# Kernel tuning notes

Measured on AMD Instinct MI355X. Metric: run time of the kernel, lower is better.

The kernel has to match this reference:

```python
import jax, jax.numpy as jnp
import numpy as np

N = 512        # n_nodes
S = 64         # state_dim
M = 64         # message_dim
HM = 128       # hidden_unit_message_dim
HR = 128       # hidden_unit_readout_dim
STEPS = 5      # n_steps


def setup_inputs() -> dict:
    key = jax.random.key(0)
    ks = jax.random.split(key, 12)
    def w(k, shape):
        return jax.random.normal(k, shape, jnp.float32) * 0.1  # normal_(0, 0.1)
    gru_bound = 1.0 / np.sqrt(S)  # torch GRUCell default init
    def u(k, shape):
        return jax.random.uniform(k, shape, jnp.float32, -gru_bound, gru_bound)
    return {
        "J": jax.random.normal(ks[0], (N, N), jnp.float32),
        "b": jax.random.normal(ks[1], (N,), jnp.float32),
        # message MLP (weights stored [in, out])
        "mW1": w(ks[2], (2 * S + 3, HM)), "mb1": jnp.zeros((HM,), jnp.float32),
        "mW2": w(ks[3], (HM, HM)),        "mb2": jnp.zeros((HM,), jnp.float32),
        "mW3": w(ks[4], (HM, M)),         "mb3": jnp.zeros((M,), jnp.float32),
        # GRUCell params (torch layout: [3*hidden, in])
        "W_ih": u(ks[5], (3 * S, M)), "b_ih": u(ks[6], (3 * S,)),
        "W_hh": u(ks[7], (3 * S, S)), "b_hh": u(ks[8], (3 * S,)),
        # readout MLP
        "rW1": w(ks[9], (S, HR)),  "rb1": jnp.zeros((HR,), jnp.float32),
        "rW2": w(ks[10], (HR, HR)), "rb2": jnp.zeros((HR,), jnp.float32),
        "rW3": w(ks[11], (HR, 2)),  "rb3": jnp.zeros((2,), jnp.float32),
    }


def reference(J, b, mW1, mb1, mW2, mb2, mW3, mb3,
              W_ih, b_ih, W_hh, b_hh,
              rW1, rb1, rW2, rb2, rW3, rb3):
    n = J.shape[0]
    # split first message layer: input = [h_i, h_j, J_ij, b_i, b_j]
    W_hi, W_hj = mW1[:S], mW1[S:2 * S]
    w_J, w_bi, w_bj = mW1[2 * S], mW1[2 * S + 1], mW1[2 * S + 2]
    # pair-dependent, state-independent part of layer-1 preactivation  [N,N,HM]
    pair_bias = (J[:, :, None] * w_J + b[:, None, None] * w_bi
                 + b[None, :, None] * w_bj + mb1)

    def gru(x, h):
        gx = x @ W_ih.T + b_ih
        gh = h @ W_hh.T + b_hh
        xr, xz, xn = jnp.split(gx, 3, axis=-1)
        hr, hz, hn = jnp.split(gh, 3, axis=-1)
        r = jax.nn.sigmoid(xr + hr)
        z = jax.nn.sigmoid(xz + hz)
        ncand = jnp.tanh(xn + r * hn)
        return (1.0 - z) * ncand + z * h

    def step(h, _):
        pre = (h @ W_hi)[:, None, :] + (h @ W_hj)[None, :, :] + pair_bias  # [N,N,HM]
        h1 = jax.nn.relu(pre)
        h2 = jax.nn.relu(h1 @ mW2 + mb2)       # [N,N,HM]
        msg_ij = h2 @ mW3 + mb3                # [N,N,M]
        msg = msg_ij.sum(axis=0)               # sum over i -> message to j  [N,M]
        return gru(msg, h), None

    h0 = jnp.zeros((n, S), J.dtype)
    hT, _ = jax.lax.scan(step, h0, None, length=STEPS)
    out = jax.nn.relu(hT @ rW1 + rb1)
    out = jax.nn.relu(out @ rW2 + rb2)
    out = out @ rW3 + rb3                      # [N,2]
    return jax.nn.softmax(out, axis=1)
```

## Files before the change

kernel.cpp:

```cpp
#include <hip/hip_runtime.h>
#include <math.h>
#include <stdint.h>

typedef _Float16 half8 __attribute__((ext_vector_type(8)));
typedef float f32x4 __attribute__((ext_vector_type(4)));
typedef float fvec4 __attribute__((ext_vector_type(4)));
typedef uint32_t u32x4 __attribute__((ext_vector_type(4)));

#define NN   512
#define SS   64
#define HMID 128
#define MM   64

__global__ void prep_all_kernel(const float* __restrict__ b,
                                const float* __restrict__ mW1,
                                const float* __restrict__ mb1,
                                const float* __restrict__ W_ih,
                                const float* __restrict__ W_hh,
                                float* __restrict__ hbuf,
                                float* __restrict__ Hi, float* __restrict__ Hj,
                                float* __restrict__ WT_ih,
                                float* __restrict__ WT_hh) {
    int idx = blockIdx.x * 256 + threadIdx.x;
    if (idx < 32768) {
        hbuf[idx] = 0.0f;
    } else if (idx < 32768 + 65536) {
        int j = idx - 32768;
        int node = j >> 7, dm = j & 127;
        float bn = b[node];
        Hi[j] = bn * mW1[129 * HMID + dm];
        Hj[j] = bn * mW1[130 * HMID + dm] + mb1[dm];
    } else if (idx < 32768 + 65536 + 12288) {
        int j = idx - 32768 - 65536;
        int g = j / 64, k = j % 64;
        WT_ih[k * 192 + g] = W_ih[j];
        WT_hh[k * 192 + g] = W_hh[j];
    }
}

__global__ __launch_bounds__(256) void main_step_kernel(
    const float* __restrict__ Hi, const float* __restrict__ Hj,
    const float* __restrict__ J, const float* __restrict__ wJ_g,
    const float* __restrict__ mW2, const float* __restrict__ mb2,
    const float* __restrict__ mW3, float* __restrict__ msg,
    float* __restrict__ partial, int use_partial) {

    __shared__ __align__(16) _Float16 H1h[2][32 * 128];
    __shared__ __align__(16) _Float16 H1l[2][32 * 128];

    const int t   = threadIdx.x;
    const int w   = t >> 6;
    const int l   = t & 63;
    const int l16 = l & 15;
    const int lg  = l >> 4;

    const int j0 = (blockIdx.x & 31) * 16;
    const int ig = blockIdx.x >> 5;

    const int lj = t >> 4;
    const int c  = t & 15;
    fvec4 hjv0 = *(const fvec4*)&Hj[(j0 + lj) * HMID + c * 8];
    fvec4 hjv1 = *(const fvec4*)&Hj[(j0 + lj) * HMID + c * 8 + 4];
    fvec4 wjv0 = *(const fvec4*)&wJ_g[c * 8];
    fvec4 wjv1 = *(const fvec4*)&wJ_g[c * 8 + 4];

    half8 w2h[2][4], w2l[2][4];
    float mb2v[2];
    #pragma unroll
    for (int nb = 0; nb < 2; ++nb) {
        int col = w * 32 + nb * 16 + l16;
        mb2v[nb] = mb2[col];
        #pragma unroll
        for (int kb = 0; kb < 4; ++kb)
            #pragma unroll
            for (int i = 0; i < 8; ++i) {
                int k = kb * 32 + lg * 8 + i;
                float wv = mW2[k * HMID + col];
                _Float16 hh = (_Float16)wv;
                w2h[nb][kb][i] = hh;
                w2l[nb][kb][i] = (_Float16)(wv - (float)hh);
            }
    }

    auto do_pre = [&](int tt, _Float16* __restrict__ dsth,
                      _Float16* __restrict__ dstl) {
        int i0 = (ig * 8 + tt) * 2;
        #pragma unroll
        for (int it = 0; it < 2; ++it) {
            int p = it * 16 + lj;
            float Jw = J[(i0 + it) * NN + j0 + lj];
            fvec4 hi0 = *(const fvec4*)&Hi[(i0 + it) * HMID + c * 8];
            fvec4 hi1 = *(const fvec4*)&Hi[(i0 + it) * HMID + c * 8 + 4];
            half8 hvh, hvl;
            #pragma unroll
            for (int u = 0; u < 4; ++u) {
                float v0 = hi0[u] + hjv0[u] + Jw * wjv0[u];
                float v1 = hi1[u] + hjv1[u] + Jw * wjv1[u];
                v0 = v0 > 0.f ? v0 : 0.f;
                v1 = v1 > 0.f ? v1 : 0.f;
                _Float16 g0 = (_Float16)v0, g1 = (_Float16)v1;
                hvh[u]     = g0;
                hvh[u + 4] = g1;
                hvl[u]     = (_Float16)(v0 - (float)g0);
                hvl[u + 4] = (_Float16)(v1 - (float)g1);
            }
            int addr = p * 128 + ((c ^ lj) << 3);
            *(half8*)&dsth[addr] = hvh;
            *(half8*)&dstl[addr] = hvl;
        }
    };

    do_pre(0, H1h[0], H1l[0]);
    __syncthreads();

    float sacc[2][4];
    #pragma unroll
    for (int nb = 0; nb < 2; ++nb)
        #pragma unroll
        for (int q = 0; q < 4; ++q) sacc[nb][q] = 0.f;

    for (int tt = 0; tt < 8; ++tt) {
        const _Float16* srch = H1h[tt & 1];
        const _Float16* srcl = H1l[tt & 1];
        if (tt < 7) do_pre(tt + 1, H1h[(tt + 1) & 1], H1l[(tt + 1) & 1]);

        f32x4 acc[2][2];
        #pragma unroll
        for (int mb = 0; mb < 2; ++mb)
            #pragma unroll
            for (int nb = 0; nb < 2; ++nb)
                acc[mb][nb] = (f32x4){0.f, 0.f, 0.f, 0.f};
        #pragma unroll
        for (int kb = 0; kb < 4; ++kb) {
            #pragma unroll
            for (int mb = 0; mb < 2; ++mb) {
                int row = mb * 16 + l16;
                int base = row * 128 + (((kb * 4 + lg) ^ l16) << 3);
                half8 ah = *(const half8*)&srch[base];
                half8 al = *(const half8*)&srcl[base];
                #pragma unroll
                for (int nb = 0; nb < 2; ++nb) {
                    acc[mb][nb] = __builtin_amdgcn_mfma_f32_16x16x32_f16(
                        ah, w2h[nb][kb], acc[mb][nb], 0, 0, 0);
                    acc[mb][nb] = __builtin_amdgcn_mfma_f32_16x16x32_f16(
                        al, w2h[nb][kb], acc[mb][nb], 0, 0, 0);
                    acc[mb][nb] = __builtin_amdgcn_mfma_f32_16x16x32_f16(
                        ah, w2l[nb][kb], acc[mb][nb], 0, 0, 0);
                }
            }
        }
        #pragma unroll
        for (int mb = 0; mb < 2; ++mb)
            #pragma unroll
            for (int nb = 0; nb < 2; ++nb)
                #pragma unroll
                for (int q = 0; q < 4; ++q) {
                    float v = acc[mb][nb][q] + mb2v[nb];
                    sacc[nb][q] += (v > 0.f ? v : 0.f);
                }
        __syncthreads();
    }

    uint32_t* S32 = (uint32_t*)&H1h[0][0];
    #pragma unroll
    for (int nb = 0; nb < 2; ++nb)
        #pragma unroll
        for (int q = 0; q < 4; ++q) {
            int j = lg * 4 + q;
            int colc = w * 32 + nb * 16 + l16;
            float s = sacc[nb][q];
            _Float16 hh = (_Float16)s;
            _Float16 ll = (_Float16)(s - (float)hh);
            uint16_t uh = __builtin_bit_cast(uint16_t, hh);
            uint16_t ul = __builtin_bit_cast(uint16_t, ll);
            S32[j * 128 + (colc ^ ((j & 7) << 2))] =
                (uint32_t)uh | ((uint32_t)ul << 16);
        }
    half8 w3h_[4], w3l_[4];
    {
        int col = w * 16 + l16;
        #pragma unroll
        for (int kb = 0; kb < 4; ++kb)
            #pragma unroll
            for (int i = 0; i < 8; ++i) {
                int k = kb * 32 + lg * 8 + i;
                float wv = mW3[k * MM + col];
                _Float16 hh = (_Float16)wv;
                w3h_[kb][i] = hh;
                w3l_[kb][i] = (_Float16)(wv - (float)hh);
            }
    }
    __syncthreads();

    f32x4 accD = (f32x4){0.f, 0.f, 0.f, 0.f};
    #pragma unroll
    for (int kb = 0; kb < 4; ++kb) {
        int row = l16;
        int sw = (row & 7) << 2;
        int cc = kb * 32 + lg * 8;
        const uint32_t* bp = &S32[row * 128];
        u32x4 A = *(const u32x4*)&bp[cc ^ sw];
        u32x4 B = *(const u32x4*)&bp[(cc + 4) ^ sw];
        union { uint32_t wd[4]; half8 hv; } Ah, Al;
        Ah.wd[0] = __builtin_amdgcn_perm(A[1], A[0], 0x05040100u);
        Ah.wd[1] = __builtin_amdgcn_perm(A[3], A[2], 0x05040100u);
        Ah.wd[2] = __builtin_amdgcn_perm(B[1], B[0], 0x05040100u);
        Ah.wd[3] = __builtin_amdgcn_perm(B[3], B[2], 0x05040100u);
        Al.wd[0] = __builtin_amdgcn_perm(A[1], A[0], 0x07060302u);
        Al.wd[1] = __builtin_amdgcn_perm(A[3], A[2], 0x07060302u);
        Al.wd[2] = __builtin_amdgcn_perm(B[1], B[0], 0x07060302u);
        Al.wd[3] = __builtin_amdgcn_perm(B[3], B[2], 0x07060302u);
        accD = __builtin_amdgcn_mfma_f32_16x16x32_f16(Ah.hv, w3h_[kb], accD,
                                                      0, 0, 0);
        accD = __builtin_amdgcn_mfma_f32_16x16x32_f16(Al.hv, w3h_[kb], accD,
                                                      0, 0, 0);
        accD = __builtin_amdgcn_mfma_f32_16x16x32_f16(Ah.hv, w3l_[kb], accD,
                                                      0, 0, 0);
    }

    {
        int m = w * 16 + l16;
        #pragma unroll
        for (int q = 0; q < 4; ++q) {
            int j = j0 + lg * 4 + q;
            if (use_partial)
                partial[ig * (NN * MM) + j * MM + m] = accD[q];
            else
                atomicAdd(&msg[j * MM + m], accD[q]);
        }
    }
}

__global__ __launch_bounds__(256) void gru_kernel(
    float* __restrict__ msg, const float* __restrict__ partial,
    const float* __restrict__ mb3,
    const float* __restrict__ WT_ih, const float* __restrict__ b_ih,
    const float* __restrict__ WT_hh, const float* __restrict__ b_hh,
    float* __restrict__ h, const float* __restrict__ bvec,
    const float* __restrict__ mW1, const float* __restrict__ mb1,
    float* __restrict__ Hi, float* __restrict__ Hj, int lastStep,
    int use_partial,
    const float* __restrict__ rW1, const float* __restrict__ rb1,
    const float* __restrict__ rW2, const float* __restrict__ rb2,
    const float* __restrict__ rW3, const float* __restrict__ rb3,
    float* __restrict__ out) {

    __shared__ float xb[64], hb[64], hnb[64];
    __shared__ float red[4][6][64];
    __shared__ float redx[4][64];
    __shared__ float o1[128], o2[128];
    int t = threadIdx.x;
    int d = t & 63;
    int p = t >> 6;
    int node = blockIdx.x;

    if (use_partial) {
        float s = 0.f;
        #pragma unroll
        for (int g = 0; g < 8; ++g)
            s += partial[(p * 8 + g) * (NN * MM) + node * MM + d];
        redx[p][d] = s;
    }
    __syncthreads();

    if (p == 0) {
        float x;
        if (use_partial) {
            x = redx[0][d] + redx[1][d] + redx[2][d] + redx[3][d]
                + 512.0f * mb3[d];
        } else {
            x = msg[node * MM + d] + 512.0f * mb3[d];
            msg[node * MM + d] = 0.0f;
        }
        xb[d] = x;
        hb[d] = h[node * SS + d];
    }
    __syncthreads();

    {
        float s0 = 0.f, s1 = 0.f, s2 = 0.f, s3 = 0.f, s4 = 0.f, s5 = 0.f;
        int k0 = p * 16;
        for (int kk = 0; kk < 16; ++kk) {
            int k = k0 + kk;
            float xk = xb[k], hk = hb[k];
            const float* wi = &WT_ih[k * 192];
            const float* wh = &WT_hh[k * 192];
            s0 += wi[d] * xk;
            s1 += wi[64 + d] * xk;
            s2 += wi[128 + d] * xk;
            s3 += wh[d] * hk;
            s4 += wh[64 + d] * hk;
            s5 += wh[128 + d] * hk;
        }
        red[p][0][d] = s0; red[p][1][d] = s1; red[p][2][d] = s2;
        red[p][3][d] = s3; red[p][4][d] = s4; red[p][5][d] = s5;
    }
    __syncthreads();

    if (p == 0) {
        float gxr = b_ih[d]       + red[0][0][d] + red[1][0][d] + red[2][0][d] + red[3][0][d];
        float gxz = b_ih[64 + d]  + red[0][1][d] + red[1][1][d] + red[2][1][d] + red[3][1][d];
        float gxn = b_ih[128 + d] + red[0][2][d] + red[1][2][d] + red[2][2][d] + red[3][2][d];
        float ghr = b_hh[d]       + red[0][3][d] + red[1][3][d] + red[2][3][d] + red[3][3][d];
        float ghz = b_hh[64 + d]  + red[0][4][d] + red[1][4][d] + red[2][4][d] + red[3][4][d];
        float ghn = b_hh[128 + d] + red[0][5][d] + red[1][5][d] + red[2][5][d] + red[3][5][d];
        float r = 1.f / (1.f + expf(-(gxr + ghr)));
        float z = 1.f / (1.f + expf(-(gxz + ghz)));
        float nc = tanhf(gxn + r * ghn);
        float hnew = (1.f - z) * nc + z * hb[d];
        h[node * SS + d] = hnew;
        hnb[d] = hnew;
    }
    __syncthreads();

    if (!lastStep) {
        int dm = t & 127;
        int half = t >> 7;
        float bn = bvec[node];
        if (half == 0) {
            float ai = bn * mW1[129 * HMID + dm];
            for (int k = 0; k < 64; ++k)
                ai += hnb[k] * mW1[k * HMID + dm];
            Hi[node * HMID + dm] = ai;
        } else {
            float aj = bn * mW1[130 * HMID + dm] + mb1[dm];
            for (int k = 0; k < 64; ++k)
                aj += hnb[k] * mW1[(64 + k) * HMID + dm];
            Hj[node * HMID + dm] = aj;
        }
    } else {
        if (t < 64) {
            for (int dd = 0; dd < 2; ++dd) {
                int dm = d + dd * 64;
                float a = rb1[dm];
                for (int k = 0; k < 64; ++k) a += hnb[k] * rW1[k * 128 + dm];
                o1[dm] = a > 0.f ? a : 0.f;
            }
        }
        __syncthreads();
        if (t < 64) {
            for (int dd = 0; dd < 2; ++dd) {
                int dm = d + dd * 64;
                float a = rb2[dm];
                for (int k = 0; k < 128; ++k) a += o1[k] * rW2[k * 128 + dm];
                o2[dm] = a > 0.f ? a : 0.f;
            }
        }
        __syncthreads();
        if (t < 64) {
            float p0 = 0.f, p1 = 0.f;
            for (int dd = 0; dd < 2; ++dd) {
                int k = d + dd * 64;
                p0 += o2[k] * rW3[k * 2 + 0];
                p1 += o2[k] * rW3[k * 2 + 1];
            }
            for (int off = 32; off; off >>= 1) {
                p0 += __shfl_xor(p0, off);
                p1 += __shfl_xor(p1, off);
            }
            if (d == 0) {
                p0 += rb3[0];
                p1 += rb3[1];
                float m = fmaxf(p0, p1);
                float e0 = expf(p0 - m), e1 = expf(p1 - m);
                float s = e0 + e1;
                out[node * 2 + 0] = e0 / s;
                out[node * 2 + 1] = e1 / s;
            }
        }
    }
}

extern "C" void kernel_launch(void* const* d_in, const int* in_sizes, int n_in,
                              void* d_out, int out_size, void* d_ws,
                              size_t ws_size, hipStream_t stream) {
    const float* J    = (const float*)d_in[0];
    const float* b    = (const float*)d_in[1];
    const float* mW1  = (const float*)d_in[2];
    const float* mb1  = (const float*)d_in[3];
    const float* mW2  = (const float*)d_in[4];
    const float* mb2  = (const float*)d_in[5];
    const float* mW3  = (const float*)d_in[6];
    const float* mb3  = (const float*)d_in[7];
    const float* W_ih = (const float*)d_in[8];
    const float* b_ih = (const float*)d_in[9];
    const float* W_hh = (const float*)d_in[10];
    const float* b_hh = (const float*)d_in[11];
    const float* rW1  = (const float*)d_in[12];
    const float* rb1  = (const float*)d_in[13];
    const float* rW2  = (const float*)d_in[14];
    const float* rb2  = (const float*)d_in[15];
    const float* rW3  = (const float*)d_in[16];
    const float* rb3  = (const float*)d_in[17];
    float* out = (float*)d_out;

    float* ws    = (float*)d_ws;
    float* hbuf  = ws;
    float* msg   = ws + 32768;
    float* Hi    = ws + 65536;
    float* Hj    = ws + 131072;
    float* WT_ih = ws + 196608;
    float* WT_hh = ws + 208896;
    float* partial = ws + 221184;
    size_t need = (221184 + 1048576) * sizeof(float);
    int use_partial = (ws_size >= need) ? 1 : 0;

    if (!use_partial)
        hipMemsetAsync(msg, 0, NN * MM * sizeof(float), stream);
    prep_all_kernel<<<432, 256, 0, stream>>>(b, mW1, mb1, W_ih, W_hh,
                                             hbuf, Hi, Hj, WT_ih, WT_hh);

    for (int s = 0; s < 5; ++s) {
        main_step_kernel<<<1024, 256, 0, stream>>>(Hi, Hj, J, mW1 + 128 * HMID,
                                                   mW2, mb2, mW3, msg,
                                                   partial, use_partial);
        gru_kernel<<<512, 256, 0, stream>>>(msg, partial, mb3, WT_ih, b_ih,
                                            WT_hh, b_hh, hbuf, b, mW1, mb1,
                                            Hi, Hj, s == 4, use_partial,
                                            rW1, rb1, rW2, rb2, rW3, rb3, out);
    }
}
```

Measured before the change: 194.3 us.

## Compute layer-1 activations directly in MFMA operand registers, drop LDS staging

```diff
diff --git a/kernel.cpp b/kernel.cpp
--- a/kernel.cpp
+++ b/kernel.cpp
@@ -45,8 +45,7 @@
     const float* __restrict__ mW3, float* __restrict__ msg,
     float* __restrict__ partial, int use_partial) {
 
-    __shared__ __align__(16) _Float16 H1h[2][32 * 128];
-    __shared__ __align__(16) _Float16 H1l[2][32 * 128];
+    __shared__ __align__(16) uint32_t S32[16 * 128];
 
     const int t   = threadIdx.x;
     const int w   = t >> 6;
@@ -57,12 +56,15 @@
     const int j0 = (blockIdx.x & 31) * 16;
     const int ig = blockIdx.x >> 5;
 
-    const int lj = t >> 4;
-    const int c  = t & 15;
-    fvec4 hjv0 = *(const fvec4*)&Hj[(j0 + lj) * HMID + c * 8];
-    fvec4 hjv1 = *(const fvec4*)&Hj[(j0 + lj) * HMID + c * 8 + 4];
-    fvec4 wjv0 = *(const fvec4*)&wJ_g[c * 8];
-    fvec4 wjv1 = *(const fvec4*)&wJ_g[c * 8 + 4];
+    fvec4 hjv[4][2], wjv[4][2];
+    #pragma unroll
+    for (int kb = 0; kb < 4; ++kb) {
+        int ko = kb * 32 + lg * 8;
+        hjv[kb][0] = *(const fvec4*)&Hj[(j0 + l16) * HMID + ko];
+        hjv[kb][1] = *(const fvec4*)&Hj[(j0 + l16) * HMID + ko + 4];
+        wjv[kb][0] = *(const fvec4*)&wJ_g[ko];
+        wjv[kb][1] = *(const fvec4*)&wJ_g[ko + 4];
+    }
 
     half8 w2h[2][4], w2l[2][4];
     float mb2v[2];
@@ -82,37 +84,6 @@
             }
     }
 
-    auto do_pre = [&](int tt, _Float16* __restrict__ dsth,
-                      _Float16* __restrict__ dstl) {
-        int i0 = (ig * 8 + tt) * 2;
-        #pragma unroll
-        for (int it = 0; it < 2; ++it) {
-            int p = it * 16 + lj;
-            float Jw = J[(i0 + it) * NN + j0 + lj];
-            fvec4 hi0 = *(const fvec4*)&Hi[(i0 + it) * HMID + c * 8];
-            fvec4 hi1 = *(const fvec4*)&Hi[(i0 + it) * HMID + c * 8 + 4];
-            half8 hvh, hvl;
-            #pragma unroll
-            for (int u = 0; u < 4; ++u) {
-                float v0 = hi0[u] + hjv0[u] + Jw * wjv0[u];
-                float v1 = hi1[u] + hjv1[u] + Jw * wjv1[u];
-                v0 = v0 > 0.f ? v0 : 0.f;
-                v1 = v1 > 0.f ? v1 : 0.f;
-                _Float16 g0 = (_Float16)v0, g1 = (_Float16)v1;
-                hvh[u]     = g0;
-                hvh[u + 4] = g1;
-                hvl[u]     = (_Float16)(v0 - (float)g0);
-                hvl[u + 4] = (_Float16)(v1 - (float)g1);
-            }
-            int addr = p * 128 + ((c ^ lj) << 3);
-            *(half8*)&dsth[addr] = hvh;
-            *(half8*)&dstl[addr] = hvl;
-        }
-    };
-
-    do_pre(0, H1h[0], H1l[0]);
-    __syncthreads();
-
     float sacc[2][4];
     #pragma unroll
     for (int nb = 0; nb < 2; ++nb)
@@ -120,9 +91,9 @@
         for (int q = 0; q < 4; ++q) sacc[nb][q] = 0.f;
 
     for (int tt = 0; tt < 8; ++tt) {
-        const _Float16* srch = H1h[tt & 1];
-        const _Float16* srcl = H1l[tt & 1];
-        if (tt < 7) do_pre(tt + 1, H1h[(tt + 1) & 1], H1l[(tt + 1) & 1]);
+        int i0 = ig * 16 + tt * 2;
+        float J0 = J[i0 * NN + j0 + l16];
+        float J1 = J[(i0 + 1) * NN + j0 + l16];
 
         f32x4 acc[2][2];
         #pragma unroll
@@ -130,25 +101,55 @@
             #pragma unroll
             for (int nb = 0; nb < 2; ++nb)
                 acc[mb][nb] = (f32x4){0.f, 0.f, 0.f, 0.f};
+
         #pragma unroll
         for (int kb = 0; kb < 4; ++kb) {
-            #pragma unroll
-            for (int mb = 0; mb < 2; ++mb) {
-                int row = mb * 16 + l16;
-                int base = row * 128 + (((kb * 4 + lg) ^ l16) << 3);
-                half8 ah = *(const half8*)&srch[base];
-                half8 al = *(const half8*)&srcl[base];
-                #pragma unroll
-                for (int nb = 0; nb < 2; ++nb) {
-                    acc[mb][nb] = __builtin_amdgcn_mfma_f32_16x16x32_f16(
-                        ah, w2h[nb][kb], acc[mb][nb], 0, 0, 0);
-                    acc[mb][nb] = __builtin_amdgcn_mfma_f32_16x16x32_f16(
-                        al, w2h[nb][kb], acc[mb][nb], 0, 0, 0);
-                    acc[mb][nb] = __builtin_amdgcn_mfma_f32_16x16x32_f16(
-                        ah, w2l[nb][kb], acc[mb][nb], 0, 0, 0);
-                }
-            }
-        }
+            int ko = kb * 32 + lg * 8;
+            fvec4 hiA0 = *(const fvec4*)&Hi[i0 * HMID + ko];
+            fvec4 hiA1 = *(const fvec4*)&Hi[i0 * HMID + ko + 4];
+            fvec4 hiB0 = *(const fvec4*)&Hi[(i0 + 1) * HMID + ko];
+            fvec4 hiB1 = *(const fvec4*)&Hi[(i0 + 1) * HMID + ko + 4];
+
+            half8 ah0, al0, ah1, al1;
+            #pragma unroll
+            for (int u = 0; u < 4; ++u) {
+                float vA0 = hiA0[u] + hjv[kb][0][u] + J0 * wjv[kb][0][u];
+                float vA1 = hiA1[u] + hjv[kb][1][u] + J0 * wjv[kb][1][u];
+                float vB0 = hiB0[u] + hjv[kb][0][u] + J1 * wjv[kb][0][u];
+                float vB1 = hiB1[u] + hjv[kb][1][u] + J1 * wjv[kb][1][u];
+                vA0 = vA0 > 0.f ? vA0 : 0.f;
+                vA1 = vA1 > 0.f ? vA1 : 0.f;
+                vB0 = vB0 > 0.f ? vB0 : 0.f;
+                vB1 = vB1 > 0.f ? vB1 : 0.f;
+                _Float16 gA0 = (_Float16)vA0, gA1 = (_Float16)vA1;
+                _Float16 gB0 = (_Float16)vB0, gB1 = (_Float16)vB1;
+                ah0[u]     = gA0;
+                ah0[u + 4] = gA1;
+                ah1[u]     = gB0;
+                ah1[u + 4] = gB1;
+                al0[u]     = (_Float16)(vA0 - (float)gA0);
+                al0[u + 4] = (_Float16)(vA1 - (float)gA1);
+                al1[u]     = (_Float16)(vB0 - (float)gB0);
+                al1[u + 4] = (_Float16)(vB1 - (float)gB1);
+            }
+
+            #pragma unroll
+            for (int nb = 0; nb < 2; ++nb) {
+                acc[0][nb] = __builtin_amdgcn_mfma_f32_16x16x32_f16(
+                    ah0, w2h[nb][kb], acc[0][nb], 0, 0, 0);
+                acc[0][nb] = __builtin_amdgcn_mfma_f32_16x16x32_f16(
+                    al0, w2h[nb][kb], acc[0][nb], 0, 0, 0);
+                acc[0][nb] = __builtin_amdgcn_mfma_f32_16x16x32_f16(
+                    ah0, w2l[nb][kb], acc[0][nb], 0, 0, 0);
+                acc[1][nb] = __builtin_amdgcn_mfma_f32_16x16x32_f16(
+                    ah1, w2h[nb][kb], acc[1][nb], 0, 0, 0);
+                acc[1][nb] = __builtin_amdgcn_mfma_f32_16x16x32_f16(
+                    al1, w2h[nb][kb], acc[1][nb], 0, 0, 0);
+                acc[1][nb] = __builtin_amdgcn_mfma_f32_16x16x32_f16(
+                    ah1, w2l[nb][kb], acc[1][nb], 0, 0, 0);
+            }
+        }
+
         #pragma unroll
         for (int mb = 0; mb < 2; ++mb)
             #pragma unroll
@@ -158,10 +159,8 @@
                     float v = acc[mb][nb][q] + mb2v[nb];
                     sacc[nb][q] += (v > 0.f ? v : 0.f);
                 }
-        __syncthreads();
-    }
-
-    uint32_t* S32 = (uint32_t*)&H1h[0][0];
+    }
+
     #pragma unroll
     for (int nb = 0; nb < 2; ++nb)
         #pragma unroll
```

New measurement: 287.2 us. 47.8% more time.

## Fuse GRU update into message kernel via last-block-done counters

Applied to the files above, without the earlier changes.

```diff
diff --git a/kernel.cpp b/kernel.cpp
--- a/kernel.cpp
+++ b/kernel.cpp
@@ -17,21 +17,26 @@
                                 const float* __restrict__ mb1,
                                 const float* __restrict__ W_ih,
                                 const float* __restrict__ W_hh,
-                                float* __restrict__ hbuf,
+                                float* __restrict__ h,
+                                float* __restrict__ msg,
+                                int* __restrict__ counters,
                                 float* __restrict__ Hi, float* __restrict__ Hj,
                                 float* __restrict__ WT_ih,
                                 float* __restrict__ WT_hh) {
     int idx = blockIdx.x * 256 + threadIdx.x;
     if (idx < 32768) {
-        hbuf[idx] = 0.0f;
-    } else if (idx < 32768 + 65536) {
-        int j = idx - 32768;
+        h[idx] = 0.0f;
+        if (idx < 160) counters[idx] = 0;
+    } else if (idx < 65536) {
+        msg[idx - 32768] = 0.0f;
+    } else if (idx < 65536 + 65536) {
+        int j = idx - 65536;
         int node = j >> 7, dm = j & 127;
         float bn = b[node];
         Hi[j] = bn * mW1[129 * HMID + dm];
         Hj[j] = bn * mW1[130 * HMID + dm] + mb1[dm];
-    } else if (idx < 32768 + 65536 + 12288) {
-        int j = idx - 32768 - 65536;
+    } else if (idx < 65536 + 65536 + 12288) {
+        int j = idx - 65536 - 65536;
         int g = j / 64, k = j % 64;
         WT_ih[k * 192 + g] = W_ih[j];
         WT_hh[k * 192 + g] = W_hh[j];
@@ -43,10 +48,22 @@
     const float* __restrict__ J, const float* __restrict__ wJ_g,
     const float* __restrict__ mW2, const float* __restrict__ mb2,
     const float* __restrict__ mW3, float* __restrict__ msg,
-    float* __restrict__ partial, int use_partial) {
-
-    __shared__ __align__(16) _Float16 H1h[2][32 * 128];
-    __shared__ __align__(16) _Float16 H1l[2][32 * 128];
+    int* __restrict__ counters, int step,
+    const float* __restrict__ mb3,
+    const float* __restrict__ WT_ih, const float* __restrict__ b_ih,
+    const float* __restrict__ WT_hh, const float* __restrict__ b_hh,
+    float* __restrict__ h, const float* __restrict__ bvec,
+    const float* __restrict__ mW1, const float* __restrict__ mb1,
+    float* __restrict__ Hi_w, float* __restrict__ Hj_w,
+    const float* __restrict__ rW1, const float* __restrict__ rb1,
+    const float* __restrict__ rW2, const float* __restrict__ rb2,
+    const float* __restrict__ rW3, const float* __restrict__ rb3,
+    float* __restrict__ out) {
+
+    __shared__ __align__(16) float smem[8192];
+    __shared__ int winFlag;
+    _Float16* H1hB = (_Float16*)smem;
+    _Float16* H1lB = (_Float16*)(smem + 4096);
 
     const int t   = threadIdx.x;
     const int w   = t >> 6;
@@ -54,7 +71,8 @@
     const int l16 = l & 15;
     const int lg  = l >> 4;
 
-    const int j0 = (blockIdx.x & 31) * 16;
+    const int jblk = blockIdx.x & 31;
+    const int j0 = jblk * 16;
     const int ig = blockIdx.x >> 5;
 
     const int lj = t >> 4;
@@ -110,7 +128,7 @@
         }
     };
 
-    do_pre(0, H1h[0], H1l[0]);
+    do_pre(0, H1hB, H1lB);
     __syncthreads();
 
     float sacc[2][4];
@@ -120,9 +138,10 @@
         for (int q = 0; q < 4; ++q) sacc[nb][q] = 0.f;
 
     for (int tt = 0; tt < 8; ++tt) {
-        const _Float16* srch = H1h[tt & 1];
-        const _Float16* srcl = H1l[tt & 1];
-        if (tt < 7) do_pre(tt + 1, H1h[(tt + 1) & 1], H1l[(tt + 1) & 1]);
+        const _Float16* srch = H1hB + (tt & 1) * 4096;
+        const _Float16* srcl = H1lB + (tt & 1) * 4096;
+        if (tt < 7) do_pre(tt + 1, H1hB + ((tt + 1) & 1) * 4096,
+                           H1lB + ((tt + 1) & 1) * 4096);
 
         f32x4 acc[2][2];
         #pragma unroll
@@ -161,7 +180,7 @@
         __syncthreads();
     }
 
-    uint32_t* S32 = (uint32_t*)&H1h[0][0];
+    uint32_t* S32 = (uint32_t*)smem;
     #pragma unroll
     for (int nb = 0; nb < 2; ++nb)
         #pragma unroll
@@ -223,149 +242,163 @@
         #pragma unroll
         for (int q = 0; q < 4; ++q) {
             int j = j0 + lg * 4 + q;
-            if (use_partial)
-                partial[ig * (NN * MM) + j * MM + m] = accD[q];
-            else
-                atomicAdd(&msg[j * MM + m], accD[q]);
-        }
-    }
-}
-
-__global__ __launch_bounds__(256) void gru_kernel(
-    float* __restrict__ msg, const float* __restrict__ partial,
-    const float* __restrict__ mb3,
-    const float* __restrict__ WT_ih, const float* __restrict__ b_ih,
-    const float* __restrict__ WT_hh, const float* __restrict__ b_hh,
-    float* __restrict__ h, const float* __restrict__ bvec,
-    const float* __restrict__ mW1, const float* __restrict__ mb1,
-    float* __restrict__ Hi, float* __restrict__ Hj, int lastStep,
-    int use_partial,
-    const float* __restrict__ rW1, const float* __restrict__ rb1,
-    const float* __restrict__ rW2, const float* __restrict__ rb2,
-    const float* __restrict__ rW3, const float* __restrict__ rb3,
-    float* __restrict__ out) {
-
-    __shared__ float xb[64], hb[64], hnb[64];
-    __shared__ float red[4][6][64];
-    __shared__ float redx[4][64];
-    __shared__ float o1[128], o2[128];
-    int t = threadIdx.x;
-    int d = t & 63;
-    int p = t >> 6;
-    int node = blockIdx.x;
-
-    if (use_partial) {
-        float s = 0.f;
-        #pragma unroll
-        for (int g = 0; g < 8; ++g)
-            s += partial[(p * 8 + g) * (NN * MM) + node * MM + d];
-        redx[p][d] = s;
-    }
-    __syncthreads();
-
-    if (p == 0) {
-        float x;
-        if (use_partial) {
-            x = redx[0][d] + redx[1][d] + redx[2][d] + redx[3][d]
-                + 512.0f * mb3[d];
-        } else {
-            x = msg[node * MM + d] + 512.0f * mb3[d];
-            msg[node * MM + d] = 0.0f;
-        }
-        xb[d] = x;
-        hb[d] = h[node * SS + d];
+            atomicAdd(&msg[j * MM + m], accD[q]);
+        }
+    }
+
+    __syncthreads();
+    if (t == 0) {
+        __threadfence();
+        int old = atomicAdd(&counters[step * 32 + jblk], 1);
+        winFlag = (old == 31) ? 1 : 0;
+    }
+    __syncthreads();
+    if (!winFlag) return;
+
+    float* xb   = smem;
+    float* hb   = smem + 1024;
+    float* hnb  = smem + 2048;
+    float* gsum = smem + 3072;
+    float* ghn  = smem + 6144;
+
+    const int n16  = t >> 4;
+    const int sl   = t & 15;
+    const int node = j0 + n16;
+
+    __syncthreads();
+    #pragma unroll
+    for (int q = 0; q < 4; ++q) {
+        int m = sl * 4 + q;
+        float v = __hip_atomic_load(&msg[node * MM + m], __ATOMIC_RELAXED,
+                                    __HIP_MEMORY_SCOPE_AGENT);
+        __hip_atomic_store(&msg[node * MM + m], 0.0f, __ATOMIC_RELAXED,
+                           __HIP_MEMORY_SCOPE_AGENT);
+        xb[n16 * 64 + m] = v + 512.0f * mb3[m];
+        hb[n16 * 64 + m] = h[node * SS + m];
     }
     __syncthreads();
 
     {
-        float s0 = 0.f, s1 = 0.f, s2 = 0.f, s3 = 0.f, s4 = 0.f, s5 = 0.f;
-        int k0 = p * 16;
-        for (int kk = 0; kk < 16; ++kk) {
-            int k = k0 + kk;
-            float xk = xb[k], hk = hb[k];
-            const float* wi = &WT_ih[k * 192];
-            const float* wh = &WT_hh[k * 192];
-            s0 += wi[d] * xk;
-            s1 += wi[64 + d] * xk;
-            s2 += wi[128 + d] * xk;
-            s3 += wh[d] * hk;
-            s4 += wh[64 + d] * hk;
-            s5 += wh[128 + d] * hk;
-        }
-        red[p][0][d] = s0; red[p][1][d] = s1; red[p][2][d] = s2;
-        red[p][3][d] = s3; red[p][4][d] = s4; red[p][5][d] = s5;
-    }
-    __syncthreads();
-
-    if (p == 0) {
-        float gxr = b_ih[d]       + red[0][0][d] + red[1][0][d] + red[2][0][d] + red[3][0][d];
-        float gxz = b_ih[64 + d]  + red[0][1][d] + red[1][1][d] + red[2][1][d] + red[3][1][d];
-        float gxn = b_ih[128 + d] + red[0][2][d] + red[1][2][d] + red[2][2][d] + red[3][2][d];
-        float ghr = b_hh[d]       + red[0][3][d] + red[1][3][d] + red[2][3][d] + red[3][3][d];
-        float ghz = b_hh[64 + d]  + red[0][4][d] + red[1][4][d] + red[2][4][d] + red[3][4][d];
-        float ghn = b_hh[128 + d] + red[0][5][d] + red[1][5][d] + red[2][5][d] + red[3][5][d];
-        float r = 1.f / (1.f + expf(-(gxr + ghr)));
-        float z = 1.f / (1.f + expf(-(gxz + ghz)));
-        float nc = tanhf(gxn + r * ghn);
-        float hnew = (1.f - z) * nc + z * hb[d];
+        float gxa[12], gha[12];
+        #pragma unroll
+        for (int e = 0; e < 12; ++e) { gxa[e] = 0.f; gha[e] = 0.f; }
+        for (int k = 0; k < 64; ++k) {
+            float xk = xb[n16 * 64 + k], hk = hb[n16 * 64 + k];
+            const float* wi = &WT_ih[k * 192 + sl * 12];
+            const float* wh = &WT_hh[k * 192 + sl * 12];
+            #pragma unroll
+            for (int e = 0; e < 12; ++e) {
+                gxa[e] += wi[e] * xk;
+                gha[e] += wh[e] * hk;
+            }
+        }
+        #pragma unroll
+        for (int e = 0; e < 12; ++e) {
+            int g = sl * 12 + e;
+            if (g < 128) {
+                gsum[n16 * 192 + g] = gxa[e] + b_ih[g] + gha[e] + b_hh[g];
+            } else {
+                gsum[n16 * 192 + g] = gxa[e] + b_ih[g];
+                ghn[n16 * 64 + (g - 128)] = gha[e] + b_hh[g];
+            }
+        }
+    }
+    __syncthreads();
+
+    #pragma unroll
+    for (int q = 0; q < 4; ++q) {
+        int d = sl * 4 + q;
+        float r  = 1.f / (1.f + expf(-gsum[n16 * 192 + d]));
+        float z  = 1.f / (1.f + expf(-gsum[n16 * 192 + 64 + d]));
+        float nc = tanhf(gsum[n16 * 192 + 128 + d] + r * ghn[n16 * 64 + d]);
+        float hnew = (1.f - z) * nc + z * hb[n16 * 64 + d];
         h[node * SS + d] = hnew;
-        hnb[d] = hnew;
-    }
-    __syncthreads();
-
-    if (!lastStep) {
-        int dm = t & 127;
-        int half = t >> 7;
+        hnb[n16 * 64 + d] = hnew;
+    }
+    __syncthreads();
+
+    if (step < 4) {
         float bn = bvec[node];
-        if (half == 0) {
-            float ai = bn * mW1[129 * HMID + dm];
-            for (int k = 0; k < 64; ++k)
-                ai += hnb[k] * mW1[k * HMID + dm];
-            Hi[node * HMID + dm] = ai;
-        } else {
-            float aj = bn * mW1[130 * HMID + dm] + mb1[dm];
-            for (int k = 0; k < 64; ++k)
-                aj += hnb[k] * mW1[(64 + k) * HMID + dm];
-            Hj[node * HMID + dm] = aj;
+        float ai[8], aj[8];
+        #pragma unroll
+        for (int e = 0; e < 8; ++e) {
+            int dm = sl * 8 + e;
+            ai[e] = bn * mW1[129 * HMID + dm];
+            aj[e] = bn * mW1[130 * HMID + dm] + mb1[dm];
+        }
+        for (int k = 0; k < 64; ++k) {
+            float hk = hnb[n16 * 64 + k];
+            const float* r1 = &mW1[k * HMID + sl * 8];
+            const float* r2 = &mW1[(64 + k) * HMID + sl * 8];
+            #pragma unroll
+            for (int e = 0; e < 8; ++e) {
+                ai[e] += hk * r1[e];
+                aj[e] += hk * r2[e];
+            }
+        }
+        #pragma unroll
+        for (int e = 0; e < 8; ++e) {
+            int dm = sl * 8 + e;
+            Hi_w[node * HMID + dm] = ai[e];
+            Hj_w[node * HMID + dm] = aj[e];
         }
     } else {
-        if (t < 64) {
-            for (int dd = 0; dd < 2; ++dd) {
-                int dm = d + dd * 64;
-                float a = rb1[dm];
-                for (int k = 0; k < 64; ++k) a += hnb[k] * rW1[k * 128 + dm];
-                o1[dm] = a > 0.f ? a : 0.f;
-            }
+        float* o1 = gsum;
+        float* o2 = smem + 5120;
+        {
+            float a8[8];
+            #pragma unroll
+            for (int e = 0; e < 8; ++e) a8[e] = rb1[sl * 8 + e];
+            for (int k = 0; k < 64; ++k) {
+                float hk = hnb[n16 * 64 + k];
+                const float* r1 = &rW1[k * 128 + sl * 8];
+                #pragma unroll
+                for (int e = 0; e < 8; ++e) a8[e] += hk * r1[e];
+            }
+            #pragma unroll
+            for (int e = 0; e < 8; ++e)
+                o1[n16 * 128 + sl * 8 + e] = a8[e] > 0.f ? a8[e] : 0.f;
         }
         __syncthreads();
-        if (t < 64) {
-            for (int dd = 0; dd < 2; ++dd) {
-                int dm = d + dd * 64;
-                float a = rb2[dm];
-                for (int k = 0; k < 128; ++k) a += o1[k] * rW2[k * 128 + dm];
-                o2[dm] = a > 0.f ? a : 0.f;
-            }
+        {
+            float a8[8];
+            #pragma unroll
+            for (int e = 0; e < 8; ++e) a8[e] = rb2[sl * 8 + e];
+            for (int k = 0; k < 128; ++k) {
+                float vk = o1[n16 * 128 + k];
+                const float* r2 = &rW2[k * 128 + sl * 8];
+                #pragma unroll
+                for (int e = 0; e < 8; ++e) a8[e] += vk * r2[e];
+            }
+            #pragma unroll
+            for (int e = 0; e < 8; ++e)
+                o2[n16 * 128 + sl * 8 + e] = a8[e] > 0.f ? a8[e] : 0.f;
         }
         __syncthreads();
-        if (t < 64) {
+        {
             float p0 = 0.f, p1 = 0.f;
-            for (int dd = 0; dd < 2; ++dd) {
-                int k = d + dd * 64;
-                p0 += o2[k] * rW3[k * 2 + 0];
-                p1 += o2[k] * rW3[k * 2 + 1];
-            }
-            for (int off = 32; off; off >>= 1) {
-                p0 += __shfl_xor(p0, off);
-                p1 += __shfl_xor(p1, off);
-            }
-            if (d == 0) {
-                p0 += rb3[0];
-                p1 += rb3[1];
-                float m = fmaxf(p0, p1);
-                float e0 = expf(p0 - m), e1 = expf(p1 - m);
-                float s = e0 + e1;
-                out[node * 2 + 0] = e0 / s;
-                out[node * 2 + 1] = e1 / s;
+            #pragma unroll
+            for (int e = 0; e < 8; ++e) {
+                int k = sl * 8 + e;
+                float vk = o2[n16 * 128 + k];
+                p0 += vk * rW3[k * 2 + 0];
+                p1 += vk * rW3[k * 2 + 1];
+            }
+            hb[n16 * 16 + sl] = p0;
+            hb[256 + n16 * 16 + sl] = p1;
+            __syncthreads();
+            if (sl == 0) {
+                float s0 = rb3[0], s1 = rb3[1];
+                #pragma unroll
+                for (int e = 0; e < 16; ++e) {
+                    s0 += hb[n16 * 16 + e];
+                    s1 += hb[256 + n16 * 16 + e];
+                }
+                float m = fmaxf(s0, s1);
+                float e0 = expf(s0 - m), e1 = expf(s1 - m);
+                float den = e0 + e1;
+                out[node * 2 + 0] = e0 / den;
+                out[node * 2 + 1] = e1 / den;
             }
         }
     }
@@ -397,26 +430,26 @@
     float* ws    = (float*)d_ws;
     float* hbuf  = ws;
     float* msg   = ws + 32768;
-    float* Hi    = ws + 65536;
-    float* Hj    = ws + 131072;
-    float* WT_ih = ws + 196608;
-    float* WT_hh = ws + 208896;
-    float* partial = ws + 221184;
-    size_t need = (221184 + 1048576) * sizeof(float);
-    int use_partial = (ws_size >= need) ? 1 : 0;
-
-    if (!use_partial)
-        hipMemsetAsync(msg, 0, NN * MM * sizeof(float), stream);
-    prep_all_kernel<<<432, 256, 0, stream>>>(b, mW1, mb1, W_ih, W_hh,
-                                             hbuf, Hi, Hj, WT_ih, WT_hh);
+    float* Hi0   = ws + 65536;
+    float* Hj0   = ws + 131072;
+    float* Hi1   = ws + 196608;
+    float* Hj1   = ws + 262144;
+    float* WT_ih = ws + 327680;
+    float* WT_hh = ws + 339968;
+    int*   counters = (int*)(ws + 352256);
+
+    prep_all_kernel<<<560, 256, 0, stream>>>(b, mW1, mb1, W_ih, W_hh,
+                                             hbuf, msg, counters,
+                                             Hi0, Hj0, WT_ih, WT_hh);
 
     for (int s = 0; s < 5; ++s) {
-        main_step_kernel<<<1024, 256, 0, stream>>>(Hi, Hj, J, mW1 + 128 * HMID,
-                                                   mW2, mb2, mW3, msg,
-                                                   partial, use_partial);
-        gru_kernel<<<512, 256, 0, stream>>>(msg, partial, mb3, WT_ih, b_ih,
-                                            WT_hh, b_hh, hbuf, b, mW1, mb1,
-                                            Hi, Hj, s == 4, use_partial,
-                                            rW1, rb1, rW2, rb2, rW3, rb3, out);
+        const float* Hi_r = (s & 1) ? Hi1 : Hi0;
+        const float* Hj_r = (s & 1) ? Hj1 : Hj0;
+        float* Hi_w = (s & 1) ? Hi0 : Hi1;
+        float* Hj_w = (s & 1) ? Hj0 : Hj1;
+        main_step_kernel<<<1024, 256, 0, stream>>>(
+            Hi_r, Hj_r, J, mW1 + 128 * HMID, mW2, mb2, mW3, msg,
+            counters, s, mb3, WT_ih, b_ih, WT_hh, b_hh, hbuf, b, mW1, mb1,
+            Hi_w, Hj_w, rW1, rb1, rW2, rb2, rW3, rb3, out);
     }
 }
```

Measured after the change: 363.5 us. 87.1% more time.
